# Kernel optimization log

Hardware: AMD Instinct MI355X
Metric: run time of the kernel (lower is better)

Reference implementation:

```python
import jax, jax.numpy as jnp
import numpy as np


def rotate_half(x):
    x1, x2 = jnp.split(x, 2, axis=-1)
    return jnp.concatenate([-x2, x1], axis=-1)


def setup_inputs() -> dict:
    key = jax.random.key(0)
    ks = jax.random.split(key, 7)
    B, L, D = 2, 2048, 2048
    H, KVH = 16, 4
    HD = D // H  # 128
    s = 0.02
    x = jax.random.normal(ks[0], (B, L, D), jnp.float32)
    # rotary tables: use realistic cos/sin of angles
    inv_freq = 1.0 / (10000.0 ** (np.arange(0, HD, 2, dtype=np.float32) / HD))
    t = np.arange(L, dtype=np.float32)
    freqs = np.outer(t, inv_freq)  # [L, HD/2]
    emb = np.concatenate([freqs, freqs], axis=-1)  # [L, HD]
    cos = jnp.asarray(np.cos(emb), jnp.float32)
    sin = jnp.asarray(np.sin(emb), jnp.float32)
    wq = jax.random.normal(ks[1], (D, H * HD), jnp.float32) * s
    wk = jax.random.normal(ks[2], (D, KVH * HD), jnp.float32) * s
    wv = jax.random.normal(ks[3], (D, KVH * HD), jnp.float32) * s
    wo = jax.random.normal(ks[4], (H * HD, D), jnp.float32) * s
    return {"x": x, "cos": cos, "sin": sin, "wq": wq, "wk": wk, "wv": wv, "wo": wo}


def reference(x, cos, sin, wq, wk, wv, wo):
    B, L, D = x.shape
    H, KVH = 16, 4
    HD = D // H
    n_rep = H // KVH
    q = (x @ wq).reshape(B, L, H, HD).transpose(0, 2, 1, 3)     # [B,H,L,hd]
    k = (x @ wk).reshape(B, L, KVH, HD).transpose(0, 2, 1, 3)   # [B,KVH,L,hd]
    v = (x @ wv).reshape(B, L, KVH, HD).transpose(0, 2, 1, 3)
    c = cos[None, None]  # [1,1,L,hd]
    s = sin[None, None]
    q = q * c + rotate_half(q) * s
    k = k * c + rotate_half(k) * s
    if n_rep > 1:
        k = jnp.repeat(k, n_rep, axis=1)
        v = jnp.repeat(v, n_rep, axis=1)
    scale = HD ** -0.5
    attn = jnp.einsum('bhqd,bhkd->bhqk', q, k) * scale  # [B,H,L,L]
    mask = jnp.triu(jnp.ones((L, L), bool), k=1)
    attn = jnp.where(mask, -jnp.inf, attn)
    attn = jax.nn.softmax(attn, axis=-1)
    out = jnp.einsum('bhqk,bhkd->bhqd', attn, v)
    out = out.transpose(0, 2, 1, 3).reshape(B, L, H * HD)
    return out @ wo
```

## Files before the change

kernel.cpp:

```cpp
#include <hip/hip_runtime.h>

typedef __attribute__((ext_vector_type(4))) float f32x4;
typedef __attribute__((ext_vector_type(8))) short s16x8;

__device__ __forceinline__ float bf2f(short b) {
  unsigned int u = ((unsigned int)(unsigned short)b) << 16;
  return __builtin_bit_cast(float, u);
}
__device__ __forceinline__ short f2bf(float f) {
  unsigned int u = __builtin_bit_cast(unsigned int, f);
  u = (u + 0x7fffu + ((u >> 16) & 1u)) >> 16;
  return (short)u;
}
__device__ __forceinline__ unsigned cvt_pk_bf16(float a, float b) {
  unsigned r;
  asm("v_cvt_pk_bf16_f32 %0, %1, %2" : "=v"(r) : "v"(a), "v"(b));
  return r;
}

__device__ __forceinline__ void async_copy16(void* lds, const void* g) {
  __builtin_amdgcn_global_load_lds((const __attribute__((address_space(1))) unsigned int*)g,
                                   (__attribute__((address_space(3))) unsigned int*)lds,
                                   16, 0, 0);
}


__global__ __launch_bounds__(256) void cvt_f32_bf16(const float* __restrict__ src,
                                                    short* __restrict__ dst, int n) {
  const int i = (blockIdx.x * 256 + threadIdx.x) * 4;
  if (i >= n) return;
  const float4 v = *(const float4*)&src[i];
  short4 o;
  o.x = f2bf(v.x); o.y = f2bf(v.y); o.z = f2bf(v.z); o.w = f2bf(v.w);
  *(short4*)&dst[i] = o;
}

__global__ __launch_bounds__(256) void transpose_cvt(const float* __restrict__ src,
                                                     short* __restrict__ dst, int R, int C) {
  __shared__ float t[32][33];
  const int c0 = blockIdx.x * 32, r0 = blockIdx.y * 32;
  const int tx = threadIdx.x & 31;
  const int ty = threadIdx.x >> 5;
#pragma unroll
  for (int i = 0; i < 4; ++i)
    t[ty + 8 * i][tx] = src[(size_t)(r0 + ty + 8 * i) * C + c0 + tx];
  __syncthreads();
#pragma unroll
  for (int i = 0; i < 4; ++i)
    dst[(size_t)(c0 + ty + 8 * i) * R + r0 + tx] = f2bf(t[tx][ty + 8 * i]);
}

__global__ __launch_bounds__(256) void transpose_v(const short* __restrict__ qkv,
                                                   short* __restrict__ vt) {
  __shared__ short t[32][33];
  const int l0 = blockIdx.x * 32;
  const int c0 = blockIdx.y * 32;
  const int b = blockIdx.z;
  const int tx = threadIdx.x & 31, ty = threadIdx.x >> 5;
#pragma unroll
  for (int i = 0; i < 4; ++i)
    t[ty + 8 * i][tx] = qkv[(size_t)(b * 2048 + l0 + ty + 8 * i) * 3072 + 2560 + c0 + tx];
  __syncthreads();
#pragma unroll
  for (int i = 0; i < 4; ++i) {
    const int c = c0 + ty + 8 * i;
    const int l = l0 + tx;
    const int kvp = (l & 63) ^ ((c & 7) << 3);
    vt[((size_t)b * 512 + c) * 2048 + (l & ~63) + kvp] = t[tx][ty + 8 * i];
  }
}


template <bool OUT_BF16>
__global__ __launch_bounds__(256) void gemm_bt(const short* __restrict__ A,
                                               const short* __restrict__ BT,
                                               void* __restrict__ Cout,
                                               int M, int N, int K) {
  __shared__ short As[128 * 32];
  __shared__ short Bs[128 * 32];
  const int tid = threadIdx.x;
  const int l = tid & 63, wid = tid >> 6;
  const int m0 = blockIdx.x * 128, n0 = blockIdx.y * 128;
  const int wr = (wid >> 1) * 64, wc = (wid & 1) * 64;
  const int lr = l & 15, lc = l >> 4;
  f32x4 acc[4][4] = {};

  for (int k0 = 0; k0 < K; k0 += 32) {
    __syncthreads();
#pragma unroll
    for (int i = 0; i < 2; ++i) {
      const int c = tid + 256 * i;
      const int row = c >> 2, kc = (c & 3) * 8;
      async_copy16((char*)As + (size_t)(i * 256 + wid * 64) * 16,
                   A + (size_t)(m0 + row) * K + k0 + kc);
      async_copy16((char*)Bs + (size_t)(i * 256 + wid * 64) * 16,
                   BT + (size_t)(n0 + row) * K + k0 + kc);
    }
    __syncthreads();
    s16x8 a[4], b[4];
#pragma unroll
    for (int m = 0; m < 4; ++m)
      a[m] = *(const s16x8*)&As[(wr + m * 16 + lr) * 32 + lc * 8];
#pragma unroll
    for (int n = 0; n < 4; ++n)
      b[n] = *(const s16x8*)&Bs[(wc + n * 16 + lr) * 32 + lc * 8];
#pragma unroll
    for (int m = 0; m < 4; ++m)
#pragma unroll
      for (int n = 0; n < 4; ++n)
        acc[m][n] = __builtin_amdgcn_mfma_f32_16x16x32_bf16(a[m], b[n], acc[m][n], 0, 0, 0);
  }

#pragma unroll
  for (int m = 0; m < 4; ++m)
#pragma unroll
    for (int n = 0; n < 4; ++n)
#pragma unroll
      for (int r = 0; r < 4; ++r) {
        const size_t row = (size_t)(m0 + wr + m * 16 + lc * 4 + r);
        const int col = n0 + wc + n * 16 + lr;
        if constexpr (OUT_BF16)
          ((short*)Cout)[row * N + col] = f2bf(acc[m][n][r]);
        else
          ((float*)Cout)[row * N + col] = acc[m][n][r];
      }
}


__global__ __launch_bounds__(256) void rope_kernel(short* __restrict__ qkv,
                                                   short* __restrict__ kswz,
                                                   const float* __restrict__ cosb,
                                                   const float* __restrict__ sinb) {
  const int idx = blockIdx.x * 256 + threadIdx.x;
  const int d = idx & 63;
  const int hh = (idx >> 6) % 20;
  const int row = idx / (64 * 20);
  const int lpos = row & 2047;
  const int col = (hh < 16) ? hh * 128 + d : 2048 + (hh - 16) * 128 + d;
  short* p = qkv + (size_t)row * 3072 + col;
  const float x1 = bf2f(p[0]);
  const float x2 = bf2f(p[64]);
  const float c = cosb[lpos * 128 + d];
  const float sn = sinb[lpos * 128 + d];
  const short o1 = f2bf(x1 * c - x2 * sn);
  const short o2 = f2bf(x2 * c + x1 * sn);
  if (hh < 16) {
    p[0] = o1;
    p[64] = o2;
  } else {
    const int b = row >> 11;
    const int kvh = hh - 16;
    short* kp = kswz + (((size_t)(b * 4 + kvh) * 2048) + lpos) * 128;
    const int sw = (lpos & 7) << 3;
    kp[d ^ sw] = o1;
    kp[(d + 64) ^ sw] = o2;
  }
}


__global__ __launch_bounds__(256) void flash_attn(const short* __restrict__ qkv,
                                                  const short* __restrict__ kswz,
                                                  const short* __restrict__ vt,
                                                  short* __restrict__ attn_out) {
  __shared__ short Ks[64 * 128];
  __shared__ short Vs[128 * 64];
  __shared__ uint2 Pb[4][16][16];
  const int tid = threadIdx.x;
  const int l = tid & 63, w = tid >> 6;
  const int lr = l & 15, lc = l >> 4;
  const int sw = (lr & 7) << 3;
  const int qpair = blockIdx.x, h = blockIdx.y, b = blockIdx.z;
  const int kvh = h >> 2;
  const short* Qg = qkv + (size_t)b * 2048 * 3072 + h * 128;
  const short* Kg = kswz + ((size_t)(b * 4 + kvh) * 2048) * 128;
  const short* Vtg = vt + ((size_t)b * 512 + kvh * 128) * 2048;
  const float SCALE2 = 0.12751744166306968f;
  s16x8 ones;
#pragma unroll
  for (int j = 0; j < 8; ++j) ones[j] = (short)0x3F80;

#pragma unroll 1
  for (int seg = 0; seg < 2; ++seg) {
    const int qt = seg ? (31 - qpair) : qpair;
    const int qbase = qt * 64 + w * 16;

    s16x8 qf[4];
#pragma unroll
    for (int dc = 0; dc < 4; ++dc) {
      qf[dc] = *(const s16x8*)&Qg[(size_t)(qbase + lr) * 3072 + dc * 32 + lc * 8];
#pragma unroll
      for (int j = 0; j < 8; ++j) qf[dc][j] = f2bf(bf2f(qf[dc][j]) * SCALE2);
    }

    f32x4 oacc[8] = {};
    f32x4 osum = {0.f, 0.f, 0.f, 0.f};
    float mrow = -__builtin_inff();
    const int nkt = qt + 1;

    for (int kt = 0; kt < nkt; ++kt) {
      const int kv0 = kt * 64;
      __syncthreads();
#pragma unroll
      for (int i = 0; i < 4; ++i) {
        async_copy16((char*)Ks + i * 4096 + w * 1024,
                     Kg + (size_t)kv0 * 128 + i * 2048 + w * 512 + l * 8);
        async_copy16((char*)Vs + i * 4096 + w * 1024,
                     Vtg + (size_t)(i * 32 + w * 8 + (l >> 3)) * 2048 + kv0 + (l & 7) * 8);
      }
      __syncthreads();

      f32x4 sacc[4] = {};
      __builtin_amdgcn_s_setprio(1);
#pragma unroll
      for (int cb = 0; cb < 4; ++cb)
#pragma unroll
        for (int dc = 0; dc < 4; ++dc) {
          const s16x8 kf = *(const s16x8*)&Ks[(cb * 16 + lr) * 128 + ((dc * 32 + lc * 8) ^ sw)];
          sacc[cb] = __builtin_amdgcn_mfma_f32_16x16x32_bf16(kf, qf[dc], sacc[cb], 0, 0, 0);
        }
      __builtin_amdgcn_s_setprio(0);

      if (kt == qt) {
        const int qrow = qbase + lr;
#pragma unroll
        for (int cb = 0; cb < 4; ++cb)
#pragma unroll
          for (int r = 0; r < 4; ++r)
            if (kv0 + cb * 16 + lc * 4 + r > qrow) sacc[cb][r] = -1e30f;
      }

      float rm = sacc[0][0];
#pragma unroll
      for (int cb = 0; cb < 4; ++cb)
#pragma unroll
        for (int r = 0; r < 4; ++r)
          if (cb | r) rm = fmaxf(rm, sacc[cb][r]);
      rm = fmaxf(rm, __shfl_xor(rm, 16, 64));
      rm = fmaxf(rm, __shfl_xor(rm, 32, 64));

      if (!__all(rm <= mrow + 8.f)) {
        const float mnew = fmaxf(mrow, rm);
        const float resc = exp2f(mrow - mnew);
        mrow = mnew;
#pragma unroll
        for (int r = 0; r < 4; ++r) {
          const float rr = __shfl(resc, (l & 48) | (((l >> 4) & 3) * 4 + r), 64);
          osum[r] *= rr;
#pragma unroll
          for (int db = 0; db < 8; ++db) oacc[db][r] *= rr;
        }
      }

#pragma unroll
      for (int cb = 0; cb < 4; ++cb) {
        const float p0 = exp2f(sacc[cb][0] - mrow);
        const float p1 = exp2f(sacc[cb][1] - mrow);
        const float p2 = exp2f(sacc[cb][2] - mrow);
        const float p3 = exp2f(sacc[cb][3] - mrow);
        uint2 u;
        u.x = cvt_pk_bf16(p0, p1);
        u.y = cvt_pk_bf16(p2, p3);
        Pb[w][lr][(4 * cb + lc) ^ (lr & 7)] = u;
      }

      __builtin_amdgcn_s_setprio(1);
#pragma unroll
      for (int kk = 0; kk < 2; ++kk) {
        const uint2 plo = Pb[w][lr][(8 * kk + 2 * lc) ^ (lr & 7)];
        const uint2 phi = Pb[w][lr][(8 * kk + 2 * lc + 1) ^ (lr & 7)];
        union { uint2 u2[2]; s16x8 v; } pu;
        pu.u2[0] = plo; pu.u2[1] = phi;
        const s16x8 pf = pu.v;
#pragma unroll
        for (int db = 0; db < 8; ++db) {
          const s16x8 vf = *(const s16x8*)&Vs[(db * 16 + lr) * 64 + ((kk * 32 + lc * 8) ^ sw)];
          oacc[db] = __builtin_amdgcn_mfma_f32_16x16x32_bf16(pf, vf, oacc[db], 0, 0, 0);
        }
        osum = __builtin_amdgcn_mfma_f32_16x16x32_bf16(pf, ones, osum, 0, 0, 0);
      }
      __builtin_amdgcn_s_setprio(0);
    }

#pragma unroll
    for (int r = 0; r < 4; ++r) {
      const float inv = 1.0f / osum[r];
      const size_t orow = (size_t)b * 2048 + qbase + lc * 4 + r;
#pragma unroll
      for (int db = 0; db < 8; ++db)
        attn_out[orow * 2048 + h * 128 + db * 16 + lr] = f2bf(oacc[db][r] * inv);
    }
  }
}


extern "C" void kernel_launch(void* const* d_in, const int* in_sizes, int n_in,
                              void* d_out, int out_size, void* d_ws, size_t ws_size,
                              hipStream_t stream) {
  const float* x    = (const float*)d_in[0];
  const float* cosb = (const float*)d_in[1];
  const float* sinb = (const float*)d_in[2];
  const float* wq   = (const float*)d_in[3];
  const float* wk   = (const float*)d_in[4];
  const float* wv   = (const float*)d_in[5];
  const float* wo   = (const float*)d_in[6];
  float* out = (float*)d_out;

  char* ws = (char*)d_ws;
  short* xb    = (short*)(ws);
  short* vtb   = (short*)(ws);
  short* kswzb = (short*)(ws + 4194304);
  short* wqkvT = (short*)(ws + 16777216);
  short* woT   = (short*)(ws + 29360128);
  short* qkvb  = (short*)(ws + 37748736);
  short* attnb = (short*)(ws + 62914560);

  cvt_f32_bf16<<<8192, 256, 0, stream>>>(x, xb, 8388608);
  transpose_cvt<<<dim3(64, 64), 256, 0, stream>>>(wq, wqkvT, 2048, 2048);
  transpose_cvt<<<dim3(16, 64), 256, 0, stream>>>(wk, wqkvT + 2048 * 2048, 2048, 512);
  transpose_cvt<<<dim3(16, 64), 256, 0, stream>>>(wv, wqkvT + 2560 * 2048, 2048, 512);
  transpose_cvt<<<dim3(64, 64), 256, 0, stream>>>(wo, woT, 2048, 2048);

  gemm_bt<true><<<dim3(32, 24), 256, 0, stream>>>(xb, wqkvT, qkvb, 4096, 3072, 2048);
  rope_kernel<<<20480, 256, 0, stream>>>(qkvb, kswzb, cosb, sinb);
  transpose_v<<<dim3(64, 16, 2), 256, 0, stream>>>(qkvb, vtb);
  flash_attn<<<dim3(16, 16, 2), 256, 0, stream>>>(qkvb, kswzb, vtb, attnb);
  gemm_bt<false><<<dim3(32, 16), 256, 0, stream>>>(attnb, woT, out, 4096, 2048, 2048);
}
```

Before: 334.5 us.

## Double-buffer K/V tiles in flash attention with async prefetch

Result: no change. 335.4 us (+0.2%).

```diff
diff --git a/kernel.cpp b/kernel.cpp
--- a/kernel.cpp
+++ b/kernel.cpp
@@ -162,9 +162,9 @@
                                                   const short* __restrict__ kswz,
                                                   const short* __restrict__ vt,
                                                   short* __restrict__ attn_out) {
-  __shared__ short Ks[64 * 128];
-  __shared__ short Vs[128 * 64];
-  __shared__ uint2 Pb[4][16][16];
+  __shared__ short Ks[2][64 * 128];
+  __shared__ short Vs[2][128 * 64];
+  __shared__ uint2 Pb[4][16][17];
   const int tid = threadIdx.x;
   const int l = tid & 63, w = tid >> 6;
   const int lr = l & 15, lc = l >> 4;
@@ -179,10 +179,25 @@
 #pragma unroll
   for (int j = 0; j < 8; ++j) ones[j] = (short)0x3F80;
 
+  const short* kbase[4];
+  const short* vbase[4];
+#pragma unroll
+  for (int i = 0; i < 4; ++i) {
+    kbase[i] = Kg + i * 2048 + w * 512 + l * 8;
+    vbase[i] = Vtg + (size_t)(i * 32 + w * 8 + (l >> 3)) * 2048 + (l & 7) * 8;
+  }
+
 #pragma unroll 1
   for (int seg = 0; seg < 2; ++seg) {
     const int qt = seg ? (31 - qpair) : qpair;
     const int qbase = qt * 64 + w * 16;
+    const int nkt = qt + 1;
+
+#pragma unroll
+    for (int i = 0; i < 4; ++i) {
+      async_copy16((char*)Ks[0] + i * 4096 + w * 1024, kbase[i]);
+      async_copy16((char*)Vs[0] + i * 4096 + w * 1024, vbase[i]);
+    }
 
     s16x8 qf[4];
 #pragma unroll
@@ -195,19 +210,27 @@
     f32x4 oacc[8] = {};
     f32x4 osum = {0.f, 0.f, 0.f, 0.f};
     float mrow = -__builtin_inff();
-    const int nkt = qt + 1;
-
+
+#pragma unroll 1
     for (int kt = 0; kt < nkt; ++kt) {
+      const int buf = kt & 1;
       const int kv0 = kt * 64;
-      __syncthreads();
-#pragma unroll
-      for (int i = 0; i < 4; ++i) {
-        async_copy16((char*)Ks + i * 4096 + w * 1024,
-                     Kg + (size_t)kv0 * 128 + i * 2048 + w * 512 + l * 8);
-        async_copy16((char*)Vs + i * 4096 + w * 1024,
-                     Vtg + (size_t)(i * 32 + w * 8 + (l >> 3)) * 2048 + kv0 + (l & 7) * 8);
-      }
-      __syncthreads();
+      if (kt + 1 < nkt) {
+        const int nkv0 = kv0 + 64;
+#pragma unroll
+        for (int i = 0; i < 4; ++i) {
+          async_copy16((char*)Ks[buf ^ 1] + i * 4096 + w * 1024, kbase[i] + (size_t)nkv0 * 128);
+          async_copy16((char*)Vs[buf ^ 1] + i * 4096 + w * 1024, vbase[i] + nkv0);
+        }
+        asm volatile("s_waitcnt vmcnt(8)" ::: "memory");
+      } else {
+        asm volatile("s_waitcnt vmcnt(0)" ::: "memory");
+      }
+      __builtin_amdgcn_sched_barrier(0);
+      __builtin_amdgcn_s_barrier();
+
+      const short* KsB = Ks[buf];
+      const short* VsB = Vs[buf];
 
       f32x4 sacc[4] = {};
       __builtin_amdgcn_s_setprio(1);
@@ -215,7 +238,7 @@
       for (int cb = 0; cb < 4; ++cb)
 #pragma unroll
         for (int dc = 0; dc < 4; ++dc) {
-          const s16x8 kf = *(const s16x8*)&Ks[(cb * 16 + lr) * 128 + ((dc * 32 + lc * 8) ^ sw)];
+          const s16x8 kf = *(const s16x8*)&KsB[(cb * 16 + lr) * 128 + ((dc * 32 + lc * 8) ^ sw)];
           sacc[cb] = __builtin_amdgcn_mfma_f32_16x16x32_bf16(kf, qf[dc], sacc[cb], 0, 0, 0);
         }
       __builtin_amdgcn_s_setprio(0);
@@ -260,25 +283,27 @@
         uint2 u;
         u.x = cvt_pk_bf16(p0, p1);
         u.y = cvt_pk_bf16(p2, p3);
-        Pb[w][lr][(4 * cb + lc) ^ (lr & 7)] = u;
+        Pb[w][lr][4 * cb + lc] = u;
       }
 
       __builtin_amdgcn_s_setprio(1);
 #pragma unroll
       for (int kk = 0; kk < 2; ++kk) {
-        const uint2 plo = Pb[w][lr][(8 * kk + 2 * lc) ^ (lr & 7)];
-        const uint2 phi = Pb[w][lr][(8 * kk + 2 * lc + 1) ^ (lr & 7)];
+        const uint2 plo = Pb[w][lr][8 * kk + 2 * lc];
+        const uint2 phi = Pb[w][lr][8 * kk + 2 * lc + 1];
         union { uint2 u2[2]; s16x8 v; } pu;
         pu.u2[0] = plo; pu.u2[1] = phi;
         const s16x8 pf = pu.v;
 #pragma unroll
         for (int db = 0; db < 8; ++db) {
-          const s16x8 vf = *(const s16x8*)&Vs[(db * 16 + lr) * 64 + ((kk * 32 + lc * 8) ^ sw)];
+          const s16x8 vf = *(const s16x8*)&VsB[(db * 16 + lr) * 64 + ((kk * 32 + lc * 8) ^ sw)];
           oacc[db] = __builtin_amdgcn_mfma_f32_16x16x32_bf16(pf, vf, oacc[db], 0, 0, 0);
         }
         osum = __builtin_amdgcn_mfma_f32_16x16x32_bf16(pf, ones, osum, 0, 0, 0);
       }
       __builtin_amdgcn_s_setprio(0);
+      __builtin_amdgcn_sched_barrier(0);
+      __builtin_amdgcn_s_barrier();
     }
 
 #pragma unroll
```
